# Performance work log

Measured on AMD Instinct MI355X. Metric: run time of the kernel, lower is better.

## Reference

```python
import jax, jax.numpy as jnp
import numpy as np

B, N, D = 16, 1024, 16  # graphs, nodes, embedding_dim


def setup_inputs() -> dict:
    key = jax.random.key(0)
    ks = jax.random.split(key, 13)
    s = 0.05  # small weight scale to keep exp(alpha) well-behaved
    return {
        "X": jax.random.normal(ks[0], (B, N, D), dtype=jnp.float32),
        "init_param": jax.random.normal(ks[1], (2,), dtype=jnp.float32) * s,
        "Wq": jax.random.normal(ks[2], (D - 1, D, D), dtype=jnp.float32) * s,
        "bq": jax.random.normal(ks[3], (D - 1, D), dtype=jnp.float32) * s,
        "Wk": jax.random.normal(ks[4], (D - 1, D, D), dtype=jnp.float32) * s,
        "bk": jax.random.normal(ks[5], (D - 1, D), dtype=jnp.float32) * s,
        "Wv": jax.random.normal(ks[6], (D - 1, D, D), dtype=jnp.float32) * s,
        "bv": jax.random.normal(ks[7], (D - 1, D), dtype=jnp.float32) * s,
        "Wo": jax.random.normal(ks[8], (D - 1, D, D), dtype=jnp.float32) * s,
        "bo": jax.random.normal(ks[9], (D - 1, D), dtype=jnp.float32) * s,
        "Wf": jax.random.normal(ks[10], (D - 1, 2, D), dtype=jnp.float32) * s,
        "bf": jax.random.normal(ks[11], (D - 1, 2), dtype=jnp.float32) * s,
    }


def reference(X, init_param, Wq, bq, Wk, bk, Wv, bv, Wo, bo, Wf, bf):
    b, n, d = X.shape
    dt = X.dtype
    Zs = []
    logdet = jnp.zeros((b, n), dt)
    for i in range(d):
        if i == 0:
            mu, alpha = init_param[0], init_param[1]
        else:
            l = i - 1
            Xi = X[:, :, :i]  # [B,N,i] growing ragged slice
            Q = Xi @ Wq[l, :i, :i].T + bq[l, :i]
            K = Xi @ Wk[l, :i, :i].T + bk[l, :i]
            V = Xi @ Wv[l, :i, :i].T + bv[l, :i]
            # SAB/MAB: softmax(QK^T / sqrt(dim_V=i)); num_heads=1
            A = jax.nn.softmax(
                jnp.einsum("bnd,bmd->bnm", Q, K) / jnp.sqrt(jnp.asarray(i, dt)),
                axis=-1,
            )  # [B,N,N]
            O = Q + jnp.einsum("bnm,bmd->bnd", A, V)
            O = O + jax.nn.relu(O @ Wo[l, :i, :i].T + bo[l, :i])
            out = O @ Wf[l, :, :i].T + bf[l]  # [B,N,2]
            mu, alpha = out[..., 0], out[..., 1]
        Zs.append((X[:, :, i] - mu) / jnp.exp(alpha))
        logdet = logdet - alpha
    Z = jnp.stack(Zs, axis=-1)
    return Z, logdet
```

## Files before the change

kernel.cpp:

```cpp
#include <hip/hip_runtime.h>
#include <math.h>

#define Bb 16
#define Nn 1024
#define Dd 16
#define NL 15

typedef __attribute__((ext_vector_type(8))) short short8;
typedef __attribute__((ext_vector_type(16))) float f32x16;
typedef __attribute__((ext_vector_type(4))) unsigned uint4v;

#if __has_builtin(__builtin_amdgcn_exp2f)
#define EXP2(x) __builtin_amdgcn_exp2f(x)
#else
#define EXP2(x) exp2f(x)
#endif

#define VSTR 1040
#define V_OFF 32768
#define ONES_OFF 66048
#define RS_OFF 69632
#define LDS_TOTAL 73728

__device__ __forceinline__ unsigned pack2bf(float a, float b) {
    unsigned ua = __float_as_uint(a) + 0x8000u;
    unsigned ub = __float_as_uint(b) + 0x8000u;
    return (ua >> 16) | (ub & 0xffff0000u);
}
__device__ __forceinline__ unsigned short bf1(float a) {
    return (unsigned short)((__float_as_uint(a) + 0x8000u) >> 16);
}

__device__ __forceinline__ unsigned expperm(float x, float y) {
    unsigned ex = __float_as_uint(EXP2(x));
    unsigned ey = __float_as_uint(EXP2(y));
#if __has_builtin(__builtin_amdgcn_perm)
    return __builtin_amdgcn_perm(ey, ex, 0x07060302);
#else
    return (ex >> 16) | (ey & 0xffff0000u);
#endif
}

__device__ __forceinline__ int vperm(int m) {
    return (m & 3) + ((m & 8) >> 1) + ((m & 4) << 1);
}

__device__ __forceinline__ void project(const float* __restrict__ xrow,
                                        const float* __restrict__ W,
                                        const float* __restrict__ bias,
                                        int i, float* __restrict__ q) {
#pragma unroll
    for (int r = 0; r < 16; r++) q[r] = 0.f;
    for (int c = 0; c < i; c++) {
        float xc = xrow[c];
#pragma unroll
        for (int r = 0; r < 16; r++) q[r] = fmaf(xc, W[r * 16 + c], q[r]);
    }
#pragma unroll
    for (int r = 0; r < 16; r++) q[r] = (r < i) ? (q[r] + bias[r]) : 0.f;
}

__device__ __forceinline__ void load_row16(const float* __restrict__ p, float* __restrict__ x) {
    const float4* xp = (const float4*)p;
    float4 a = xp[0], b = xp[1], c = xp[2], d = xp[3];
    x[0]=a.x; x[1]=a.y; x[2]=a.z; x[3]=a.w;
    x[4]=b.x; x[5]=b.y; x[6]=b.z; x[7]=b.w;
    x[8]=c.x; x[9]=c.y; x[10]=c.z; x[11]=c.w;
    x[12]=d.x; x[13]=d.y; x[14]=d.z; x[15]=d.w;
}

__launch_bounds__(1024, 4)
__global__ void gf_fused(const float* __restrict__ X, const float* __restrict__ ip,
                         const float* __restrict__ Wq, const float* __restrict__ bq,
                         const float* __restrict__ Wk, const float* __restrict__ bk,
                         const float* __restrict__ Wv, const float* __restrict__ bv,
                         const float* __restrict__ Wo, const float* __restrict__ bo,
                         const float* __restrict__ Wf, const float* __restrict__ bf,
                         float* __restrict__ out) {
    extern __shared__ char smem[];
    const int l = blockIdx.x, b = blockIdx.y, i = l + 1;
    const int t = threadIdx.x;
    const int wid = t >> 6, lane = t & 63;
    const int q31 = lane & 31, h = lane >> 5;
    const float qscale = 1.4426950408889634f * rsqrtf((float)i);

    unsigned short* Ksh  = (unsigned short*)smem;
    unsigned short* Vsh  = (unsigned short*)(smem + V_OFF);
    unsigned short* Ones = (unsigned short*)(smem + ONES_OFF);

    const float* Xb  = X  + (size_t)b * Nn * Dd;
    const float* wq  = Wq + l * 256;  const float* bql = bq + l * 16;
    const float* wk  = Wk + l * 256;  const float* bkl = bk + l * 16;
    const float* wvp = Wv + l * 256;  const float* bvl = bv + l * 16;
    const float* wo  = Wo + l * 256;  const float* bol = bo + l * 16;
    const float* wf  = Wf + l * 32;   const float* bfl = bf + l * 2;

    unsigned qu[8];
    {
        float xr[16]; load_row16(Xb + (size_t)t * Dd, xr);
        float tmp[16];

        project(xr, wk, bkl, i, tmp);
        {
            unsigned u[8];
#pragma unroll
            for (int r = 0; r < 8; r++) u[r] = pack2bf(tmp[2*r], tmp[2*r+1]);
            uint4* kd = (uint4*)(Ksh + t * 16);
            kd[0] = make_uint4(u[0], u[1], u[2], u[3]);
            kd[1] = make_uint4(u[4], u[5], u[6], u[7]);
        }

        project(xr, wvp, bvl, i, tmp);
        {
            unsigned short* vcol = Vsh + (t & ~15) + vperm(t & 15);
#pragma unroll
            for (int d = 0; d < 16; d++) vcol[d * VSTR] = bf1(tmp[d]);
        }

        Ones[t] = 0x3F80;

        project(xr, wq, bql, i, tmp);
#pragma unroll
        for (int r = 0; r < 8; r++) qu[r] = pack2bf(tmp[2*r] * qscale, tmp[2*r+1] * qscale);
    }
    __syncthreads();

    short8 qf0, qf1;
    {
        unsigned d0[4], d1[4];
#pragma unroll
        for (int j = 0; j < 4; j++) {
            unsigned lo = __shfl(qu[j], q31);
            unsigned hi = __shfl(qu[4 + j], q31);
            d0[j] = h ? hi : lo;
            lo = __shfl(qu[j], 32 + q31);
            hi = __shfl(qu[4 + j], 32 + q31);
            d1[j] = h ? hi : lo;
        }
        uint4v v0 = {d0[0], d0[1], d0[2], d0[3]};
        uint4v v1 = {d1[0], d1[1], d1[2], d1[3]};
        qf0 = __builtin_bit_cast(short8, v0);
        qf1 = __builtin_bit_cast(short8, v1);
    }

    f32x16 zf16 = {};
    f32x16 D0 = {}, D1 = {};

    const unsigned short* Kp = Ksh + (size_t)q31 * 16 + h * 8;
    const unsigned short* Vp = ((q31 < 16) ? (Vsh + (size_t)q31 * VSTR) : Ones) + 8 * h;

    short8 kf  = *(const short8*)Kp;
    short8 vc0 = *(const short8*)(Vp);
    short8 vc1 = *(const short8*)(Vp + 16);

#pragma unroll 2
    for (int kb = 0; kb < Nn; kb += 32) {
        const int kn = (kb + 32) & (Nn - 1);
        short8 kfn = *(const short8*)(Kp + (size_t)kn * 16);
        short8 vn0 = *(const short8*)(Vp + kn);
        short8 vn1 = *(const short8*)(Vp + kn + 16);

        f32x16 s0 = __builtin_amdgcn_mfma_f32_32x32x16_bf16(kf, qf0, zf16, 0, 0, 0);
        f32x16 s1 = __builtin_amdgcn_mfma_f32_32x32x16_bf16(kf, qf1, zf16, 0, 0, 0);
        kf = kfn;

        {
            uint4v a0 = {expperm(s0[0], s0[1]), expperm(s0[2], s0[3]),
                         expperm(s0[4], s0[5]), expperm(s0[6], s0[7])};
            D0 = __builtin_amdgcn_mfma_f32_32x32x16_bf16(
                     __builtin_bit_cast(short8, a0), vc0, D0, 0, 0, 0);
            uint4v a1 = {expperm(s1[0], s1[1]), expperm(s1[2], s1[3]),
                         expperm(s1[4], s1[5]), expperm(s1[6], s1[7])};
            D1 = __builtin_amdgcn_mfma_f32_32x32x16_bf16(
                     __builtin_bit_cast(short8, a1), vc0, D1, 0, 0, 0);
        }
        {
            uint4v a0 = {expperm(s0[8], s0[9]),  expperm(s0[10], s0[11]),
                         expperm(s0[12], s0[13]), expperm(s0[14], s0[15])};
            D0 = __builtin_amdgcn_mfma_f32_32x32x16_bf16(
                     __builtin_bit_cast(short8, a0), vc1, D0, 0, 0, 0);
            uint4v a1 = {expperm(s1[8], s1[9]),  expperm(s1[10], s1[11]),
                         expperm(s1[12], s1[13]), expperm(s1[14], s1[15])};
            D1 = __builtin_amdgcn_mfma_f32_32x32x16_bf16(
                     __builtin_bit_cast(short8, a1), vc1, D1, 0, 0, 0);
        }
        vc0 = vn0; vc1 = vn1;
    }

    __syncthreads();

    float* Ow = (float*)smem + wid * (64 * 17);
    if (q31 < 16) {
#pragma unroll
        for (int r = 0; r < 16; r++) {
            int m = (r & 3) + 8 * (r >> 2) + 4 * h;
            Ow[m * 17 + q31]        = D0[r];
            Ow[(m + 32) * 17 + q31] = D1[r];
        }
    }
    float* Rw = (float*)(smem + RS_OFF) + wid * 64;
    if (q31 == 16) {
#pragma unroll
        for (int r = 0; r < 16; r++) {
            int m = (r & 3) + 8 * (r >> 2) + 4 * h;
            Rw[m]      = D0[r];
            Rw[32 + m] = D1[r];
        }
    }

    {
        const float invq = 0.6931471805599453f * sqrtf((float)i);

        float a[16];
#pragma unroll
        for (int r = 0; r < 8; r++) {
            a[2*r]     = __uint_as_float(qu[r] << 16) * invq;
            a[2*r + 1] = __uint_as_float(qu[r] & 0xffff0000u) * invq;
        }

        const float* orow = (const float*)smem + wid * (64 * 17) + lane * 17;
        const float  inv  = 1.f / Rw[lane];
#pragma unroll
        for (int c = 0; c < 16; c++) a[c] += orow[c] * inv;

        float tt[16];
#pragma unroll
        for (int r = 0; r < 16; r++) {
            float acc = bol[r];
#pragma unroll
            for (int c = 0; c < 16; c++) acc = fmaf(a[c], wo[r * 16 + c], acc);
            tt[r] = fmaxf(acc, 0.f);
        }
#pragma unroll
        for (int r = 0; r < 16; r++) a[r] += (r < i) ? tt[r] : 0.f;

        float mu = bfl[0], al = bfl[1];
#pragma unroll
        for (int c = 0; c < 16; c++) {
            mu = fmaf(a[c], wf[c], mu);
            al = fmaf(a[c], wf[16 + c], al);
        }
        const float xi = Xb[(size_t)t * Dd + i];
        out[((size_t)(b * Nn + t)) * Dd + i] = (xi - mu) * __expf(-al);

        float ldadd = al;
        if (l == 0) {
            const float mu0 = ip[0], a0 = ip[1];
            const float x0 = Xb[(size_t)t * Dd];
            out[((size_t)(b * Nn + t)) * Dd] = (x0 - mu0) * __expf(-a0);
            ldadd += a0;
        }
        atomicAdd(out + (size_t)Bb * Nn * Dd + b * Nn + t, -ldadd);
    }
}

__global__ void gf_init(const float* __restrict__ X, const float* __restrict__ ip,
                        float* __restrict__ out) {
    int idx = blockIdx.x * blockDim.x + threadIdx.x;
    if (idx >= Bb * Nn) return;
    float mu = ip[0], alpha = ip[1];
    float x0 = X[(size_t)idx * Dd];
    out[(size_t)idx * Dd] = (x0 - mu) * __expf(-alpha);
    out[(size_t)Bb * Nn * Dd + idx] = -alpha;
}

__launch_bounds__(512, 2)
__global__ void gf_layer_fb(const float* __restrict__ X,
                            const float* __restrict__ Wq, const float* __restrict__ bq,
                            const float* __restrict__ Wk, const float* __restrict__ bk,
                            const float* __restrict__ Wv, const float* __restrict__ bv,
                            const float* __restrict__ Wo, const float* __restrict__ bo,
                            const float* __restrict__ Wf, const float* __restrict__ bf,
                            float* __restrict__ out) {
    const int l = blockIdx.x, b = blockIdx.y, i = l + 1, t = threadIdx.x;
    const float rscale = rsqrtf((float)i);
    __shared__ float Ksh[512 * 16];
    __shared__ float Vsh[512 * 16];
    const float* Xb = X + (size_t)b * Nn * Dd;
    const float* wq = Wq + l * 256; const float* wk = Wk + l * 256;
    const float* wv = Wv + l * 256; const float* wo = Wo + l * 256;
    const float* wf = Wf + l * 32;
    const float* bql = bq + l * 16; const float* bkl = bk + l * 16;
    const float* bvl = bv + l * 16; const float* bol = bo + l * 16;
    const float* bfl = bf + l * 2;
    const int n0 = t, n1 = t + 512;
    float q0[16], q1[16], xi0, xi1;
    {
        float xr[16];
        load_row16(Xb + (size_t)n0 * Dd, xr); xi0 = xr[i]; project(xr, wq, bql, i, q0);
        load_row16(Xb + (size_t)n1 * Dd, xr); xi1 = xr[i]; project(xr, wq, bql, i, q1);
    }
    float o0[16], o1[16];
#pragma unroll
    for (int c = 0; c < 16; c++) { o0[c] = 0.f; o1[c] = 0.f; }
    float ls0 = 0.f, ls1 = 0.f;
    for (int ch = 0; ch < 2; ch++) {
        float kr[16], vr[16];
        {
            float kx[16];
            load_row16(Xb + (size_t)(ch * 512 + t) * Dd, kx);
            project(kx, wk, bkl, i, kr);
            project(kx, wv, bvl, i, vr);
        }
        __syncthreads();
#pragma unroll
        for (int j = 0; j < 4; j++) {
            ((float4*)&Ksh[t * 16])[j] = ((float4*)kr)[j];
            ((float4*)&Vsh[t * 16])[j] = ((float4*)vr)[j];
        }
        __syncthreads();
        for (int k = 0; k < 512; k++) {
            float kk[16], vv[16];
#pragma unroll
            for (int j = 0; j < 4; j++) ((float4*)kk)[j] = ((const float4*)&Ksh[k * 16])[j];
            float s0 = 0.f, s1 = 0.f;
#pragma unroll
            for (int c = 0; c < 16; c++) { s0 = fmaf(q0[c], kk[c], s0); s1 = fmaf(q1[c], kk[c], s1); }
            float p0 = __expf(s0 * rscale), p1 = __expf(s1 * rscale);
            ls0 += p0; ls1 += p1;
#pragma unroll
            for (int j = 0; j < 4; j++) ((float4*)vv)[j] = ((const float4*)&Vsh[k * 16])[j];
#pragma unroll
            for (int c = 0; c < 16; c++) { o0[c] = fmaf(p0, vv[c], o0[c]); o1[c] = fmaf(p1, vv[c], o1[c]); }
        }
        __syncthreads();
    }
    float* logdet = out + (size_t)Bb * Nn * Dd;
#pragma unroll
    for (int rowsel = 0; rowsel < 2; rowsel++) {
        const float* qr = rowsel ? q1 : q0; const float* orr = rowsel ? o1 : o0;
        float lsum = rowsel ? ls1 : ls0; float xin = rowsel ? xi1 : xi0;
        int n = rowsel ? n1 : n0;
        float a[16]; float inv = 1.f / lsum;
#pragma unroll
        for (int c = 0; c < 16; c++) a[c] = qr[c] + orr[c] * inv;
        float tt[16];
#pragma unroll
        for (int r = 0; r < 16; r++) {
            float acc = bol[r];
#pragma unroll
            for (int c = 0; c < 16; c++) acc = fmaf(a[c], wo[r * 16 + c], acc);
            tt[r] = fmaxf(acc, 0.f);
        }
#pragma unroll
        for (int r = 0; r < 16; r++) a[r] += (r < i) ? tt[r] : 0.f;
        float mu = bfl[0], al = bfl[1];
#pragma unroll
        for (int c = 0; c < 16; c++) { mu = fmaf(a[c], wf[c], mu); al = fmaf(a[c], wf[16 + c], al); }
        out[((size_t)(b * Nn + n)) * Dd + i] = (xin - mu) * __expf(-al);
        atomicAdd(logdet + b * Nn + n, -al);
    }
}

extern "C" void kernel_launch(void* const* d_in, const int* in_sizes, int n_in,
                              void* d_out, int out_size, void* d_ws, size_t ws_size,
                              hipStream_t stream) {
    const float* X  = (const float*)d_in[0];
    const float* ip = (const float*)d_in[1];
    const float* Wq = (const float*)d_in[2];
    const float* bq = (const float*)d_in[3];
    const float* Wk = (const float*)d_in[4];
    const float* bk = (const float*)d_in[5];
    const float* Wv = (const float*)d_in[6];
    const float* bv = (const float*)d_in[7];
    const float* Wo = (const float*)d_in[8];
    const float* bo = (const float*)d_in[9];
    const float* Wf = (const float*)d_in[10];
    const float* bf = (const float*)d_in[11];
    float* out = (float*)d_out;

    hipMemsetAsync(out + (size_t)Bb * Nn * Dd, 0, (size_t)Bb * Nn * sizeof(float), stream);

    hipError_t e = hipFuncSetAttribute((const void*)gf_fused,
                                       hipFuncAttributeMaxDynamicSharedMemorySize,
                                       LDS_TOTAL);
    if (e == hipSuccess) {
        gf_fused<<<dim3(NL, Bb), 1024, LDS_TOTAL, stream>>>(
            X, ip, Wq, bq, Wk, bk, Wv, bv, Wo, bo, Wf, bf, out);
    } else {
        gf_init<<<(Bb * Nn + 255) / 256, 256, 0, stream>>>(X, ip, out);
        gf_layer_fb<<<dim3(NL, Bb), 512, 0, stream>>>(
            X, Wq, bq, Wk, bk, Wv, bv, Wo, bo, Wf, bf, out);
    }
}
```

Before: 134.2 us.

## Compute softmax row sums in VALU, XOR-swizzle V in LDS, fit 64KB static LDS

Row sums of the exponentiated scores are now accumulated in registers with a cross-half shuffle, instead of being computed by the MFMA from an extra ones column. This lets the padded V layout and the ones buffer go away. V is stored in an XOR-swizzled layout that avoids bank conflicts without padding. The O staging buffer is packed to bf16, so the kernel fits in 64KB of static shared memory with no dynamic-LDS attribute call, and the fallback kernels are removed. It adds VALU adds per tile and loses some precision in O staging.

```diff
diff --git a/kernel.cpp b/kernel.cpp
--- a/kernel.cpp
+++ b/kernel.cpp
@@ -16,11 +16,6 @@
 #define EXP2(x) exp2f(x)
 #endif
 
-#define VSTR 1040
-#define V_OFF 32768
-#define ONES_OFF 66048
-#define RS_OFF 69632
-#define LDS_TOTAL 73728
 
 __device__ __forceinline__ unsigned pack2bf(float a, float b) {
     unsigned ua = __float_as_uint(a) + 0x8000u;
@@ -31,13 +26,11 @@
     return (unsigned short)((__float_as_uint(a) + 0x8000u) >> 16);
 }
 
-__device__ __forceinline__ unsigned expperm(float x, float y) {
-    unsigned ex = __float_as_uint(EXP2(x));
-    unsigned ey = __float_as_uint(EXP2(y));
+__device__ __forceinline__ unsigned permpk(float x, float y) {
 #if __has_builtin(__builtin_amdgcn_perm)
-    return __builtin_amdgcn_perm(ey, ex, 0x07060302);
+    return __builtin_amdgcn_perm(__float_as_uint(y), __float_as_uint(x), 0x07060302);
 #else
-    return (ex >> 16) | (ey & 0xffff0000u);
+    return (__float_as_uint(x) >> 16) | (__float_as_uint(y) & 0xffff0000u);
 #endif
 }
 
@@ -77,16 +70,15 @@
                          const float* __restrict__ Wo, const float* __restrict__ bo,
                          const float* __restrict__ Wf, const float* __restrict__ bf,
                          float* __restrict__ out) {
-    extern __shared__ char smem[];
+    __shared__ char smem[65536];
     const int l = blockIdx.x, b = blockIdx.y, i = l + 1;
     const int t = threadIdx.x;
     const int wid = t >> 6, lane = t & 63;
     const int q31 = lane & 31, h = lane >> 5;
     const float qscale = 1.4426950408889634f * rsqrtf((float)i);
 
-    unsigned short* Ksh  = (unsigned short*)smem;
-    unsigned short* Vsh  = (unsigned short*)(smem + V_OFF);
-    unsigned short* Ones = (unsigned short*)(smem + ONES_OFF);
+    unsigned short* Ksh = (unsigned short*)smem;
+    unsigned short* Vsh = (unsigned short*)(smem + 32768);
 
     const float* Xb  = X  + (size_t)b * Nn * Dd;
     const float* wq  = Wq + l * 256;  const float* bql = bq + l * 16;
@@ -112,12 +104,12 @@
 
         project(xr, wvp, bvl, i, tmp);
         {
-            unsigned short* vcol = Vsh + (t & ~15) + vperm(t & 15);
-#pragma unroll
-            for (int d = 0; d < 16; d++) vcol[d * VSTR] = bf1(tmp[d]);
-        }
-
-        Ones[t] = 0x3F80;
+            const int col = (t & ~15) | vperm(t & 15);
+            const int cg = col >> 3, c7 = col & 7;
+#pragma unroll
+            for (int d = 0; d < 16; d++)
+                Vsh[d * 1024 + ((cg ^ d) << 3) + c7] = bf1(tmp[d]);
+        }
 
         project(xr, wq, bql, i, tmp);
 #pragma unroll
@@ -145,68 +137,75 @@
 
     f32x16 zf16 = {};
     f32x16 D0 = {}, D1 = {};
+    float rs0 = 0.f, rs1 = 0.f;
 
     const unsigned short* Kp = Ksh + (size_t)q31 * 16 + h * 8;
-    const unsigned short* Vp = ((q31 < 16) ? (Vsh + (size_t)q31 * VSTR) : Ones) + 8 * h;
+    const int dv = q31 & 15;
+    const unsigned short* Vrow = Vsh + dv * 1024;
 
     short8 kf  = *(const short8*)Kp;
-    short8 vc0 = *(const short8*)(Vp);
-    short8 vc1 = *(const short8*)(Vp + 16);
+    short8 vc0 = *(const short8*)(Vrow + (((0 + h) ^ dv) << 3));
+    short8 vc1 = *(const short8*)(Vrow + (((2 + h) ^ dv) << 3));
 
 #pragma unroll 2
     for (int kb = 0; kb < Nn; kb += 32) {
         const int kn = (kb + 32) & (Nn - 1);
+        const int gn = (kn >> 3) + h;
         short8 kfn = *(const short8*)(Kp + (size_t)kn * 16);
-        short8 vn0 = *(const short8*)(Vp + kn);
-        short8 vn1 = *(const short8*)(Vp + kn + 16);
+        short8 vn0 = *(const short8*)(Vrow + ((gn ^ dv) << 3));
+        short8 vn1 = *(const short8*)(Vrow + (((gn + 2) ^ dv) << 3));
 
         f32x16 s0 = __builtin_amdgcn_mfma_f32_32x32x16_bf16(kf, qf0, zf16, 0, 0, 0);
         f32x16 s1 = __builtin_amdgcn_mfma_f32_32x32x16_bf16(kf, qf1, zf16, 0, 0, 0);
         kf = kfn;
 
         {
-            uint4v a0 = {expperm(s0[0], s0[1]), expperm(s0[2], s0[3]),
-                         expperm(s0[4], s0[5]), expperm(s0[6], s0[7])};
+            float e0 = EXP2(s0[0]), e1 = EXP2(s0[1]), e2 = EXP2(s0[2]), e3 = EXP2(s0[3]);
+            float e4 = EXP2(s0[4]), e5 = EXP2(s0[5]), e6 = EXP2(s0[6]), e7 = EXP2(s0[7]);
+            rs0 += ((e0 + e1) + (e2 + e3)) + ((e4 + e5) + (e6 + e7));
+            uint4v a0 = {permpk(e0, e1), permpk(e2, e3), permpk(e4, e5), permpk(e6, e7)};
             D0 = __builtin_amdgcn_mfma_f32_32x32x16_bf16(
                      __builtin_bit_cast(short8, a0), vc0, D0, 0, 0, 0);
-            uint4v a1 = {expperm(s1[0], s1[1]), expperm(s1[2], s1[3]),
-                         expperm(s1[4], s1[5]), expperm(s1[6], s1[7])};
+            e0 = EXP2(s1[0]); e1 = EXP2(s1[1]); e2 = EXP2(s1[2]); e3 = EXP2(s1[3]);
+            e4 = EXP2(s1[4]); e5 = EXP2(s1[5]); e6 = EXP2(s1[6]); e7 = EXP2(s1[7]);
+            rs1 += ((e0 + e1) + (e2 + e3)) + ((e4 + e5) + (e6 + e7));
+            uint4v a1 = {permpk(e0, e1), permpk(e2, e3), permpk(e4, e5), permpk(e6, e7)};
             D1 = __builtin_amdgcn_mfma_f32_32x32x16_bf16(
                      __builtin_bit_cast(short8, a1), vc0, D1, 0, 0, 0);
         }
         {
-            uint4v a0 = {expperm(s0[8], s0[9]),  expperm(s0[10], s0[11]),
-                         expperm(s0[12], s0[13]), expperm(s0[14], s0[15])};
+            float e0 = EXP2(s0[8]),  e1 = EXP2(s0[9]),  e2 = EXP2(s0[10]), e3 = EXP2(s0[11]);
+            float e4 = EXP2(s0[12]), e5 = EXP2(s0[13]), e6 = EXP2(s0[14]), e7 = EXP2(s0[15]);
+            rs0 += ((e0 + e1) + (e2 + e3)) + ((e4 + e5) + (e6 + e7));
+            uint4v a0 = {permpk(e0, e1), permpk(e2, e3), permpk(e4, e5), permpk(e6, e7)};
             D0 = __builtin_amdgcn_mfma_f32_32x32x16_bf16(
                      __builtin_bit_cast(short8, a0), vc1, D0, 0, 0, 0);
-            uint4v a1 = {expperm(s1[8], s1[9]),  expperm(s1[10], s1[11]),
-                         expperm(s1[12], s1[13]), expperm(s1[14], s1[15])};
+            e0 = EXP2(s1[8]);  e1 = EXP2(s1[9]);  e2 = EXP2(s1[10]); e3 = EXP2(s1[11]);
+            e4 = EXP2(s1[12]); e5 = EXP2(s1[13]); e6 = EXP2(s1[14]); e7 = EXP2(s1[15]);
+            rs1 += ((e0 + e1) + (e2 + e3)) + ((e4 + e5) + (e6 + e7));
+            uint4v a1 = {permpk(e0, e1), permpk(e2, e3), permpk(e4, e5), permpk(e6, e7)};
             D1 = __builtin_amdgcn_mfma_f32_32x32x16_bf16(
                      __builtin_bit_cast(short8, a1), vc1, D1, 0, 0, 0);
         }
         vc0 = vn0; vc1 = vn1;
     }
 
+    rs0 += __shfl_xor(rs0, 32);
+    rs1 += __shfl_xor(rs1, 32);
+
     __syncthreads();
 
-    float* Ow = (float*)smem + wid * (64 * 17);
+    unsigned* Opw = (unsigned*)((unsigned short*)smem + wid * 1024);
     if (q31 < 16) {
 #pragma unroll
-        for (int r = 0; r < 16; r++) {
+        for (int r = 0; r < 16; r += 2) {
             int m = (r & 3) + 8 * (r >> 2) + 4 * h;
-            Ow[m * 17 + q31]        = D0[r];
-            Ow[(m + 32) * 17 + q31] = D1[r];
-        }
-    }
-    float* Rw = (float*)(smem + RS_OFF) + wid * 64;
-    if (q31 == 16) {
-#pragma unroll
-        for (int r = 0; r < 16; r++) {
-            int m = (r & 3) + 8 * (r >> 2) + 4 * h;
-            Rw[m]      = D0[r];
-            Rw[32 + m] = D1[r];
-        }
-    }
+            Opw[q31 * 32 + (m >> 1)]      = pack2bf(D0[r], D0[r + 1]);
+            Opw[q31 * 32 + 16 + (m >> 1)] = pack2bf(D1[r], D1[r + 1]);
+        }
+    }
+    float* Rw = (float*)(smem + 32768) + wid * 64;
+    if (h == 0) { Rw[q31] = rs0; Rw[32 + q31] = rs1; }
 
     {
         const float invq = 0.6931471805599453f * sqrtf((float)i);
@@ -218,10 +217,13 @@
             a[2*r + 1] = __uint_as_float(qu[r] & 0xffff0000u) * invq;
         }
 
-        const float* orow = (const float*)smem + wid * (64 * 17) + lane * 17;
-        const float  inv  = 1.f / Rw[lane];
-#pragma unroll
-        for (int c = 0; c < 16; c++) a[c] += orow[c] * inv;
+        const unsigned short* Osh16 = (const unsigned short*)smem + wid * 1024;
+        const float inv = 1.f / Rw[lane];
+#pragma unroll
+        for (int d = 0; d < 16; d++) {
+            float ov = __uint_as_float((unsigned)Osh16[d * 64 + lane] << 16);
+            a[d] += ov * inv;
+        }
 
         float tt[16];
 #pragma unroll
@@ -251,104 +253,6 @@
             ldadd += a0;
         }
         atomicAdd(out + (size_t)Bb * Nn * Dd + b * Nn + t, -ldadd);
-    }
-}
-
-__global__ void gf_init(const float* __restrict__ X, const float* __restrict__ ip,
-                        float* __restrict__ out) {
-    int idx = blockIdx.x * blockDim.x + threadIdx.x;
-    if (idx >= Bb * Nn) return;
-    float mu = ip[0], alpha = ip[1];
-    float x0 = X[(size_t)idx * Dd];
-    out[(size_t)idx * Dd] = (x0 - mu) * __expf(-alpha);
-    out[(size_t)Bb * Nn * Dd + idx] = -alpha;
-}
-
-__launch_bounds__(512, 2)
-__global__ void gf_layer_fb(const float* __restrict__ X,
-                            const float* __restrict__ Wq, const float* __restrict__ bq,
-                            const float* __restrict__ Wk, const float* __restrict__ bk,
-                            const float* __restrict__ Wv, const float* __restrict__ bv,
-                            const float* __restrict__ Wo, const float* __restrict__ bo,
-                            const float* __restrict__ Wf, const float* __restrict__ bf,
-                            float* __restrict__ out) {
-    const int l = blockIdx.x, b = blockIdx.y, i = l + 1, t = threadIdx.x;
-    const float rscale = rsqrtf((float)i);
-    __shared__ float Ksh[512 * 16];
-    __shared__ float Vsh[512 * 16];
-    const float* Xb = X + (size_t)b * Nn * Dd;
-    const float* wq = Wq + l * 256; const float* wk = Wk + l * 256;
-    const float* wv = Wv + l * 256; const float* wo = Wo + l * 256;
-    const float* wf = Wf + l * 32;
-    const float* bql = bq + l * 16; const float* bkl = bk + l * 16;
-    const float* bvl = bv + l * 16; const float* bol = bo + l * 16;
-    const float* bfl = bf + l * 2;
-    const int n0 = t, n1 = t + 512;
-    float q0[16], q1[16], xi0, xi1;
-    {
-        float xr[16];
-        load_row16(Xb + (size_t)n0 * Dd, xr); xi0 = xr[i]; project(xr, wq, bql, i, q0);
-        load_row16(Xb + (size_t)n1 * Dd, xr); xi1 = xr[i]; project(xr, wq, bql, i, q1);
-    }
-    float o0[16], o1[16];
-#pragma unroll
-    for (int c = 0; c < 16; c++) { o0[c] = 0.f; o1[c] = 0.f; }
-    float ls0 = 0.f, ls1 = 0.f;
-    for (int ch = 0; ch < 2; ch++) {
-        float kr[16], vr[16];
-        {
-            float kx[16];
-            load_row16(Xb + (size_t)(ch * 512 + t) * Dd, kx);
-            project(kx, wk, bkl, i, kr);
-            project(kx, wv, bvl, i, vr);
-        }
-        __syncthreads();
-#pragma unroll
-        for (int j = 0; j < 4; j++) {
-            ((float4*)&Ksh[t * 16])[j] = ((float4*)kr)[j];
-            ((float4*)&Vsh[t * 16])[j] = ((float4*)vr)[j];
-        }
-        __syncthreads();
-        for (int k = 0; k < 512; k++) {
-            float kk[16], vv[16];
-#pragma unroll
-            for (int j = 0; j < 4; j++) ((float4*)kk)[j] = ((const float4*)&Ksh[k * 16])[j];
-            float s0 = 0.f, s1 = 0.f;
-#pragma unroll
-            for (int c = 0; c < 16; c++) { s0 = fmaf(q0[c], kk[c], s0); s1 = fmaf(q1[c], kk[c], s1); }
-            float p0 = __expf(s0 * rscale), p1 = __expf(s1 * rscale);
-            ls0 += p0; ls1 += p1;
-#pragma unroll
-            for (int j = 0; j < 4; j++) ((float4*)vv)[j] = ((const float4*)&Vsh[k * 16])[j];
-#pragma unroll
-            for (int c = 0; c < 16; c++) { o0[c] = fmaf(p0, vv[c], o0[c]); o1[c] = fmaf(p1, vv[c], o1[c]); }
-        }
-        __syncthreads();
-    }
-    float* logdet = out + (size_t)Bb * Nn * Dd;
-#pragma unroll
-    for (int rowsel = 0; rowsel < 2; rowsel++) {
-        const float* qr = rowsel ? q1 : q0; const float* orr = rowsel ? o1 : o0;
-        float lsum = rowsel ? ls1 : ls0; float xin = rowsel ? xi1 : xi0;
-        int n = rowsel ? n1 : n0;
-        float a[16]; float inv = 1.f / lsum;
-#pragma unroll
-        for (int c = 0; c < 16; c++) a[c] = qr[c] + orr[c] * inv;
-        float tt[16];
-#pragma unroll
-        for (int r = 0; r < 16; r++) {
-            float acc = bol[r];
-#pragma unroll
-            for (int c = 0; c < 16; c++) acc = fmaf(a[c], wo[r * 16 + c], acc);
-            tt[r] = fmaxf(acc, 0.f);
-        }
-#pragma unroll
-        for (int r = 0; r < 16; r++) a[r] += (r < i) ? tt[r] : 0.f;
-        float mu = bfl[0], al = bfl[1];
-#pragma unroll
-        for (int c = 0; c < 16; c++) { mu = fmaf(a[c], wf[c], mu); al = fmaf(a[c], wf[16 + c], al); }
-        out[((size_t)(b * Nn + n)) * Dd + i] = (xin - mu) * __expf(-al);
-        atomicAdd(logdet + b * Nn + n, -al);
     }
 }
 
@@ -371,15 +275,6 @@
 
     hipMemsetAsync(out + (size_t)Bb * Nn * Dd, 0, (size_t)Bb * Nn * sizeof(float), stream);
 
-    hipError_t e = hipFuncSetAttribute((const void*)gf_fused,
-                                       hipFuncAttributeMaxDynamicSharedMemorySize,
-                                       LDS_TOTAL);
-    if (e == hipSuccess) {
-        gf_fused<<<dim3(NL, Bb), 1024, LDS_TOTAL, stream>>>(
-            X, ip, Wq, bq, Wk, bk, Wv, bv, Wo, bo, Wf, bf, out);
-    } else {
-        gf_init<<<(Bb * Nn + 255) / 256, 256, 0, stream>>>(X, ip, out);
-        gf_layer_fb<<<dim3(NL, Bb), 512, 0, stream>>>(
-            X, Wq, bq, Wk, bk, Wv, bv, Wo, bo, Wf, bf, out);
-    }
-}
+    gf_fused<<<dim3(NL, Bb), 1024, 0, stream>>>(
+        X, ip, Wq, bq, Wk, bk, Wv, bv, Wo, bo, Wf, bf, out);
+}
```

New measurement: 139.8 us. 1.04x slower.
